# Optimization experiments

Measured on AMD Instinct MI355X. Metric: run time of the kernel, lower is better.

The kernel has to match this reference:

```python
import jax, jax.numpy as jnp
import numpy as np

H = 4096        # hidden_size
NH = 32         # num query heads
NG = 8          # num query groups (kv heads)
HD = H // NH    # head size = 128
B, S = 2, 2048


def gen_rope_cache(seq_length, n_elem, base=10000.0):
    theta = 1.0 / base ** (jnp.arange(0, n_elem, 2, dtype=jnp.float32) / n_elem)
    idx_theta = jnp.outer(jnp.arange(seq_length, dtype=jnp.float32), theta)
    return jnp.stack([jnp.cos(idx_theta), jnp.sin(idx_theta)], axis=-1)  # [S, n_elem//2, 2]


def apply_rope(x, cache):
    # x: [B, S, nh, hd], cache: [S, hd//2, 2]; rot_dim == hd (no pass-through)
    b, s, nh, hd = x.shape
    xr = x.reshape(b, s, nh, hd // 2, 2)
    c = cache[:s].reshape(1, s, 1, hd // 2, 2)
    out = jnp.stack([
        xr[..., 0] * c[..., 0] - xr[..., 1] * c[..., 1],
        xr[..., 1] * c[..., 0] + xr[..., 0] * c[..., 1],
    ], axis=-1)
    return out.reshape(b, s, nh, hd)


def setup_inputs() -> dict:
    key = jax.random.key(0)
    k1, k2, k3, k4 = jax.random.split(key, 4)
    x = jax.random.normal(k1, (B, S, H), dtype=jnp.float32)
    W_qkv = jax.random.normal(k2, (H, H + 2 * NG * HD), dtype=jnp.float32) * 0.02
    b_qkv = jax.random.normal(k3, (H + 2 * NG * HD,), dtype=jnp.float32) * 0.02
    W_dense = jax.random.normal(k4, (H, H), dtype=jnp.float32) * 0.02
    rope_cache = gen_rope_cache(S, HD)
    return {"x": x, "rope_cache": rope_cache, "W_qkv": W_qkv, "b_qkv": b_qkv, "W_dense": W_dense}


def reference(x, rope_cache, W_qkv, b_qkv, W_dense):
    b, s, h = x.shape
    qkv = jnp.einsum('bsh,ho->bso', x, W_qkv) + b_qkv
    q, k, v = jnp.split(qkv, [h, h + NG * HD], axis=-1)
    q = q.reshape(b, s, NH, HD)
    k = k.reshape(b, s, NG, HD)
    v = v.reshape(b, s, NG, HD)
    q = apply_rope(q, rope_cache)
    k = apply_rope(k, rope_cache)
    # GQA: group query heads [B, G, rep, S, D] against kv [B, G, S, D]
    rep = NH // NG
    qg = q.transpose(0, 2, 1, 3).reshape(b, NG, rep, s, HD)
    kg = k.transpose(0, 2, 1, 3)  # [B, G, S, D]
    vg = v.transpose(0, 2, 1, 3)
    scale = 1.0 / jnp.sqrt(jnp.float32(HD))
    scores = jnp.einsum('bgrqd,bgkd->bgrqk', qg, kg) * scale
    causal = jnp.tril(jnp.ones((s, s), dtype=bool))
    scores = jnp.where(causal, scores, jnp.float32(-1e30))
    attn = jax.nn.softmax(scores, axis=-1)
    out = jnp.einsum('bgrqk,bgkd->bgrqd', attn, vg)  # [B, G, rep, S, D]
    out = out.reshape(b, NH, s, HD).transpose(0, 2, 1, 3).reshape(b, s, h)
    return jnp.einsum('bsh,ho->bso', out, W_dense)
```

## Files before the change

### kernel.cpp

```cpp
#include <hip/hip_runtime.h>
#include <hip/hip_bf16.h>
#include <math.h>

#define BS   4096
#define HH   4096
#define NH   32
#define NG   8
#define HD   128
#define SEQ  2048
#define NQKV 6144

typedef float f32x4 __attribute__((ext_vector_type(4)));
typedef float f32x16 __attribute__((ext_vector_type(16)));
typedef short s16x8 __attribute__((ext_vector_type(8)));
typedef short s16x4 __attribute__((ext_vector_type(4)));
typedef unsigned int u32x4 __attribute__((ext_vector_type(4)));

__device__ __forceinline__ unsigned short f2bf(float f) {
  unsigned int u = __builtin_bit_cast(unsigned int, f);
  unsigned int r = (u + 0x7fffu + ((u >> 16) & 1u)) >> 16;
  return (unsigned short)r;
}
__device__ __forceinline__ float b2f(short h) {
  unsigned int u = ((unsigned int)(unsigned short)h) << 16;
  return __builtin_bit_cast(float, u);
}

__device__ __forceinline__ void gload16(const void* g, void* l) {
  __builtin_amdgcn_global_load_lds((__attribute__((address_space(1))) void*)(g),
                                   (__attribute__((address_space(3))) void*)(l), 16, 0, 0);
}

#define BARRIER __builtin_amdgcn_s_barrier()
#define PRIO1 __builtin_amdgcn_s_setprio(1)
#define PRIO0 __builtin_amdgcn_s_setprio(0)

__global__ void cast_f32_bf16(const float* __restrict__ in, short* __restrict__ out, long n4) {
  long i = (long)blockIdx.x * blockDim.x + threadIdx.x;
  long stride = (long)gridDim.x * blockDim.x;
  for (; i < n4; i += stride) {
    float4 v = *(const float4*)&in[i * 4];
    s16x4 o;
    o[0] = (short)f2bf(v.x); o[1] = (short)f2bf(v.y);
    o[2] = (short)f2bf(v.z); o[3] = (short)f2bf(v.w);
    *(s16x4*)&out[i * 4] = o;
  }
}

__global__ __launch_bounds__(256) void transpose_cast(const float* __restrict__ in,
                                                      short* __restrict__ out, int R, int C) {
  __shared__ float tile[32][33];
  int tx = threadIdx.x & 31, ty = threadIdx.x >> 5;
  long c0 = (long)blockIdx.x * 32, r0 = (long)blockIdx.y * 32;
#pragma unroll
  for (int j = 0; j < 32; j += 8)
    tile[ty + j][tx] = in[(r0 + ty + j) * C + c0 + tx];
  __syncthreads();
  int q = threadIdx.x & 7;
  int jj = threadIdx.x >> 3;
  s16x4 o;
  o[0] = (short)f2bf(tile[4 * q + 0][jj]);
  o[1] = (short)f2bf(tile[4 * q + 1][jj]);
  o[2] = (short)f2bf(tile[4 * q + 2][jj]);
  o[3] = (short)f2bf(tile[4 * q + 3][jj]);
  *(s16x4*)&out[(c0 + jj) * R + r0 + 4 * q] = o;
}

#define LDA_FR(BASE, DB)                                                         \
  {                                                                              \
    _Pragma("unroll") for (int mf = 0; mf < 4; ++mf)                             \
      _Pragma("unroll") for (int ks = 0; ks < 2; ++ks)                           \
        af[mf][ks] = *(const s16x8*)&lds[(BASE) + (DB) * 8192 + aoff[mf][ks]];   \
  }
#define LDB_FR(BASE, DB)                                                         \
  {                                                                              \
    _Pragma("unroll") for (int nf = 0; nf < 2; ++nf)                             \
      _Pragma("unroll") for (int ks = 0; ks < 2; ++ks)                           \
        bf[nf][ks] = *(const s16x8*)&lds[(BASE) + (DB) * 8192 + boff[nf][ks]];   \
  }
#define MF_Q(MS, NS)                                                             \
  {                                                                              \
    _Pragma("unroll") for (int ks = 0; ks < 2; ++ks)                             \
      _Pragma("unroll") for (int mf = 0; mf < 4; ++mf)                           \
        _Pragma("unroll") for (int nf = 0; nf < 2; ++nf)                         \
          acc[(MS) * 4 + mf][(NS) * 2 + nf] = __builtin_amdgcn_mfma_f32_16x16x32_bf16( \
              af[mf][ks], bf[nf][ks], acc[(MS) * 4 + mf][(NS) * 2 + nf], 0, 0, 0);     \
  }
#define STG_AU0(DB, KB) { gload16(sA0 + (KB), &lds[0 + (DB) * 8192 + du0]);            \
                          gload16(sA1 + (KB), &lds[0 + (DB) * 8192 + du1]); }
#define STG_BU0(DB, KB) { gload16(sB0 + (KB), &lds[32768 + (DB) * 8192 + du0]);        \
                          gload16(sB1 + (KB), &lds[32768 + (DB) * 8192 + du1]); }
#define STG_AU1(DB, KB) { gload16(sA0 + 64 * (long)K + (KB), &lds[16384 + (DB) * 8192 + du0]); \
                          gload16(sA1 + 64 * (long)K + (KB), &lds[16384 + (DB) * 8192 + du1]); }
#define STG_BU1(DB, KB) { gload16(sB0 + 32 * (long)K + (KB), &lds[49152 + (DB) * 8192 + du0]); \
                          gload16(sB1 + 32 * (long)K + (KB), &lds[49152 + (DB) * 8192 + du1]); }

#define TILE256(DB, KBS)                                                         \
  LDA_FR(0, DB); LDB_FR(32768, DB);                                              \
  STG_AU0(DB ^ 1, KBS); STG_BU0(DB ^ 1, KBS);                                    \
  BARRIER;                                                                       \
  PRIO1; MF_Q(0, 0); PRIO0;                                                      \
  asm volatile("s_waitcnt vmcnt(6)" ::: "memory");                               \
  BARRIER;                                                                       \
  LDB_FR(49152, DB);                                                             \
  STG_BU1(DB ^ 1, KBS);                                                          \
  BARRIER;                                                                       \
  PRIO1; MF_Q(0, 1); PRIO0;                                                      \
  asm volatile("s_waitcnt vmcnt(6)" ::: "memory");                               \
  BARRIER;                                                                       \
  LDA_FR(16384, DB);                                                             \
  STG_AU1(DB ^ 1, KBS);                                                          \
  BARRIER;                                                                       \
  PRIO1; MF_Q(1, 1); PRIO0;                                                      \
  BARRIER;                                                                       \
  LDB_FR(32768, DB);                                                             \
  BARRIER;                                                                       \
  PRIO1; MF_Q(1, 0); PRIO0;                                                      \
  asm volatile("s_waitcnt vmcnt(4)" ::: "memory");                               \
  BARRIER;

template <int MODE>
__global__ __launch_bounds__(512, 1) void gemm256(const short* __restrict__ A,
                                                  const short* __restrict__ Bt,
                                                  const float* __restrict__ bias,
                                                  void* __restrict__ Cout,
                                                  const float* __restrict__ cache,
                                                  short* __restrict__ Qb,
                                                  int M, int N, int K) {
  extern __shared__ short lds[];
  const int t = threadIdx.x;
  const int lane = t & 63, w = t >> 6;
  const int g = lane >> 4, lr = lane & 15;
  const int wm = w >> 2, wn = w & 3;
  const long bm = (long)blockIdx.y * 256;
  const long bn = (long)blockIdx.x * 256;

  const short *sA0, *sA1, *sB0, *sB1;
  {
    int c0 = t, c1 = t + 512;
    int h0 = c0 >> 9, r0 = (c0 >> 3) & 63, tc0 = (c0 & 7) ^ (r0 & 7);
    int h1 = c1 >> 9, r1 = (c1 >> 3) & 63, tc1 = (c1 & 7) ^ (r1 & 7);
    sA0 = A + (bm + h0 * 128 + r0) * (long)K + tc0 * 8;
    sA1 = A + (bm + h1 * 128 + r1) * (long)K + tc1 * 8;
    int g0 = c0 >> 8, rb0 = (c0 >> 3) & 31, tb0 = (c0 & 7) ^ (rb0 & 7);
    int g1 = c1 >> 8, rb1 = (c1 >> 3) & 31, tb1 = (c1 & 7) ^ (rb1 & 7);
    sB0 = Bt + (bn + g0 * 64 + rb0) * (long)K + tb0 * 8;
    sB1 = Bt + (bn + g1 * 64 + rb1) * (long)K + tb1 * 8;
  }
  const int du0 = w * 512;
  const int du1 = w * 512 + 4096;

  int aoff[4][2], boff[2][2];
#pragma unroll
  for (int mf = 0; mf < 4; ++mf)
#pragma unroll
    for (int ks = 0; ks < 2; ++ks)
      aoff[mf][ks] = wm * 4096 + (mf * 16 + lr) * 64 + (((ks * 4 + g) ^ (lr & 7)) * 8);
#pragma unroll
  for (int nf = 0; nf < 2; ++nf)
#pragma unroll
    for (int ks = 0; ks < 2; ++ks)
      boff[nf][ks] = wn * 2048 + (nf * 16 + lr) * 64 + (((ks * 4 + g) ^ (lr & 7)) * 8);

  f32x4 acc[8][4] = {};
  s16x8 af[4][2], bf[2][2];

  STG_AU0(0, 0); STG_BU0(0, 0); STG_AU1(0, 0); STG_BU1(0, 0);
  asm volatile("s_waitcnt vmcnt(0)" ::: "memory");
  BARRIER;

  const int NT = K >> 6;
  for (int kt = 0; kt < NT; kt += 2) {
    const long kb1 = (long)(kt + 1) * 64;
    const long kb2 = (kt + 2 < NT) ? (long)(kt + 2) * 64 : 0l;
    TILE256(0, kb1);
    TILE256(1, kb2);
  }

  if (MODE == 0) {
#pragma unroll
    for (int am = 0; am < 8; ++am) {
      long row = bm + wm * 128 + am * 16 + g * 4;
#pragma unroll
      for (int an = 0; an < 4; ++an) {
        long col = bn + wn * 64 + an * 16 + lr;
#pragma unroll
        for (int r = 0; r < 4; ++r)
          ((float*)Cout)[(row + r) * N + col] = acc[am][an][r];
      }
    }
  } else {
    const float scq = 0.12751743f;
#pragma unroll
    for (int am = 0; am < 8; ++am) {
      int row0 = (int)bm + wm * 128 + am * 16 + g * 4;
      int s0 = row0 & (SEQ - 1);
      int bb = row0 >> 11;
#pragma unroll
      for (int an = 0; an < 4; ++an) {
        int col = (int)bn + wn * 64 + an * 16 + lr;
        float bv = bias[col];
        int h = col >> 7, d = col & 127;
        const int odd = lr & 1;
#pragma unroll
        for (int r = 0; r < 4; ++r) {
          float v = acc[am][an][r] + bv;
          float p = __shfl_xor(v, 1);
          float2 cs = *(const float2*)&cache[((long)(s0 + r) * 64 + (d >> 1)) * 2];
          float o = odd ? (v * cs.x + p * cs.y) : (v * cs.x - p * cs.y);
          Qb[((long)(bb * NH + h) * SEQ + s0 + r) * HD + d] = (short)f2bf(o * scq);
        }
      }
    }
  }
}

#define KV_LDA(MSB, DB, KS)                                                      \
  { _Pragma("unroll") for (int mf = 0; mf < 4; ++mf)                             \
      af[mf] = *(const s16x8*)&lds[(MSB) + (DB) * 8192 + aoff[mf][KS]]; }
#define KV_LDB(DB, KS)                                                           \
  { _Pragma("unroll") for (int nf = 0; nf < 2; ++nf)                             \
      bfk[nf] = *(const s16x8*)&lds[32768 + (DB) * 8192 + boff[nf][KS]]; }
#define KV_MF(MS)                                                                \
  { _Pragma("unroll") for (int mf = 0; mf < 4; ++mf)                             \
      _Pragma("unroll") for (int nf = 0; nf < 2; ++nf)                           \
        acc[(MS) * 4 + mf][nf] = __builtin_amdgcn_mfma_f32_16x16x32_bf16(        \
            af[mf], bfk[nf], acc[(MS) * 4 + mf][nf], 0, 0, 0); }
#define KV_SA0(DB, KB) { gload16(sA0 + (KB), &lds[(DB) * 8192 + du0]);                 \
                         gload16(sA1 + (KB), &lds[(DB) * 8192 + du1]); }
#define KV_SA1(DB, KB) { gload16(sA0 + 64 * (long)HH + (KB), &lds[16384 + (DB) * 8192 + du0]); \
                         gload16(sA1 + 64 * (long)HH + (KB), &lds[16384 + (DB) * 8192 + du1]); }
#define KV_SB(DB, KB)  { gload16(sB0 + (KB), &lds[32768 + (DB) * 8192 + du0]);         \
                         gload16(sB1 + (KB), &lds[32768 + (DB) * 8192 + du1]); }

#define KVTILE(DB, KBS)                                                          \
  KV_LDA(0, DB, 0); KV_LDB(DB, 0);                                               \
  KV_SA0(DB ^ 1, KBS);                                                           \
  BARRIER;                                                                       \
  PRIO1; KV_MF(0); PRIO0;                                                        \
  asm volatile("s_waitcnt vmcnt(2)" ::: "memory");                               \
  BARRIER;                                                                       \
  KV_LDA(16384, DB, 0);                                                          \
  KV_SB(DB ^ 1, KBS);                                                            \
  BARRIER;                                                                       \
  PRIO1; KV_MF(1); PRIO0;                                                        \
  BARRIER;                                                                       \
  KV_LDA(16384, DB, 1); KV_LDB(DB, 1);                                           \
  KV_SA1(DB ^ 1, KBS);                                                           \
  BARRIER;                                                                       \
  PRIO1; KV_MF(1); PRIO0;                                                        \
  BARRIER;                                                                       \
  KV_LDA(0, DB, 1);                                                              \
  BARRIER;                                                                       \
  PRIO1; KV_MF(0); PRIO0;                                                        \
  asm volatile("s_waitcnt vmcnt(2)" ::: "memory");                               \
  BARRIER;

__global__ __launch_bounds__(512, 1) void gemm_kv(const short* __restrict__ A,
                                                  const short* __restrict__ Bt,
                                                  const float* __restrict__ bias,
                                                  const float* __restrict__ cache,
                                                  short* __restrict__ Kb,
                                                  short* __restrict__ Vtb) {
  extern __shared__ short lds[];
  const int t = threadIdx.x;
  const int lane = t & 63, w = t >> 6;
  const int g = lane >> 4, lr = lane & 15;
  const int wm = w >> 2, wn = w & 3;
  const long bm = (long)blockIdx.y * 256;
  const int bnl = blockIdx.x * 128;

  const short *sA0, *sA1, *sB0, *sB1;
  {
    int c0 = t, c1 = t + 512;
    int h0 = c0 >> 9, r0 = (c0 >> 3) & 63, tc0 = (c0 & 7) ^ (r0 & 7);
    int h1 = c1 >> 9, r1 = (c1 >> 3) & 63, tc1 = (c1 & 7) ^ (r1 & 7);
    sA0 = A + (bm + h0 * 128 + r0) * (long)HH + tc0 * 8;
    sA1 = A + (bm + h1 * 128 + r1) * (long)HH + tc1 * 8;
    int rb0 = c0 >> 3, tb0 = (c0 & 7) ^ (rb0 & 7);
    int rb1 = c1 >> 3, tb1 = (c1 & 7) ^ (rb1 & 7);
    sB0 = Bt + ((long)bnl + rb0) * HH + tb0 * 8;
    sB1 = Bt + ((long)bnl + rb1) * HH + tb1 * 8;
  }
  const int du0 = w * 512;
  const int du1 = w * 512 + 4096;

  int aoff[4][2], boff[2][2];
#pragma unroll
  for (int mf = 0; mf < 4; ++mf)
#pragma unroll
    for (int ks = 0; ks < 2; ++ks)
      aoff[mf][ks] = wm * 4096 + (mf * 16 + lr) * 64 + (((ks * 4 + g) ^ (lr & 7)) * 8);
#pragma unroll
  for (int nf = 0; nf < 2; ++nf)
#pragma unroll
    for (int ks = 0; ks < 2; ++ks)
      boff[nf][ks] = wn * 2048 + (nf * 16 + lr) * 64 + (((ks * 4 + g) ^ (lr & 7)) * 8);

  f32x4 acc[8][2] = {};
  s16x8 af[4], bfk[2];

  KV_SA0(0, 0); KV_SB(0, 0); KV_SA1(0, 0);
  asm volatile("s_waitcnt vmcnt(0)" ::: "memory");
  BARRIER;

  for (int kt = 0; kt < 64; kt += 2) {
    const long kb1 = (long)(kt + 1) * 64;
    const long kb2 = (kt + 2 < 64) ? (long)(kt + 2) * 64 : 0l;
    KVTILE(0, kb1);
    KVTILE(1, kb2);
  }

#pragma unroll
  for (int am = 0; am < 8; ++am) {
    int row0 = (int)bm + wm * 128 + am * 16 + g * 4;
    int s0 = row0 & (SEQ - 1);
    int bb = row0 >> 11;
#pragma unroll
    for (int an = 0; an < 2; ++an) {
      int cl = bnl + wn * 32 + an * 16 + lr;
      float bv = bias[4096 + cl];
      if (cl < 1024) {
        int gi = cl >> 7, d = cl & 127;
        const int odd = lr & 1;
#pragma unroll
        for (int r = 0; r < 4; ++r) {
          float v = acc[am][an][r] + bv;
          float p = __shfl_xor(v, 1);
          float2 cs = *(const float2*)&cache[((long)(s0 + r) * 64 + (d >> 1)) * 2];
          float o = odd ? (v * cs.x + p * cs.y) : (v * cs.x - p * cs.y);
          Kb[((long)(bb * NG + gi) * SEQ + s0 + r) * HD + d] = (short)f2bf(o);
        }
      } else {
        int cv = cl - 1024;
        int gi = cv >> 7, d = cv & 127;
        s16x4 o;
#pragma unroll
        for (int r = 0; r < 4; ++r) o[r] = (short)f2bf(acc[am][an][r] + bv);
        *(s16x4*)&Vtb[((long)(bb * NG + gi) * HD + d) * SEQ + s0] = o;
      }
    }
  }
}

__global__ __launch_bounds__(512, 1) void attn(const short* __restrict__ Qb,
                                               const short* __restrict__ Kb,
                                               const short* __restrict__ Vtb,
                                               short* __restrict__ Ob) {
  extern __shared__ short alds[];
  const int t = threadIdx.x, lane = t & 63, w = t >> 6;
  const int l31 = lane & 31, hi = lane >> 5;
  const int bid = (int)blockIdx.x;
  const int q0 = (bid >> 1) & 3;
  const int qt = ((bid ^ (bid >> 8)) & 1) ? 7 - q0 : q0;
  const int head = (bid >> 3) & 63;
  const int b = head >> 5, h = head & 31;
  const int qb = qt * 256;
  const short* Qhead = Qb + (long)(b * NH + h) * SEQ * HD;
  const short* Khead = Kb + (long)(b * NG + (h >> 2)) * SEQ * HD;
  const short* Vthead = Vtb + (long)(b * NG + (h >> 2)) * SEQ * HD;
  const int qw0 = qb + w * 32;
  const int qrow = qw0 + l31;
  float* facs = (float*)&alds[32768] + w * 32;

  s16x8 qf[8];
#pragma unroll
  for (int ds = 0; ds < 8; ++ds)
    qf[ds] = *(const s16x8*)&Qhead[(long)qrow * HD + ds * 16 + hi * 8];

  const short *kp0, *kp1, *vp0, *vp1;
  {
    int c0 = t, c1 = t + 512;
    int kr0 = c0 >> 4, kc0 = (c0 & 15) ^ (kr0 & 15);
    int kr1 = c1 >> 4, kc1 = (c1 & 15) ^ (kr1 & 15);
    kp0 = Khead + (long)kr0 * HD + kc0 * 8;
    kp1 = Khead + (long)kr1 * HD + kc1 * 8;
    int vr0 = c0 >> 3, vc0 = (c0 & 7) ^ (vr0 & 7);
    int vr1 = c1 >> 3, vc1 = (c1 & 7) ^ (vr1 & 7);
    vp0 = Vthead + (long)vr0 * SEQ + vc0 * 8;
    vp1 = Vthead + (long)vr1 * SEQ + vc1 * 8;
  }
  const int d0 = w * 512, d1 = w * 512 + 4096;

  f32x16 ao[4] = {};
  float mrun = -1.0e30f, lrun = 0.0f;
  const int nkt = 4 * qt + 4;

  gload16(kp0, &alds[d0]); gload16(kp1, &alds[d1]);
  gload16(vp0, &alds[16384 + d0]); gload16(vp1, &alds[16384 + d1]);
  kp0 += 64 * HD; kp1 += 64 * HD; vp0 += 64; vp1 += 64;
  asm volatile("s_waitcnt vmcnt(0)" ::: "memory");
  BARRIER;

  for (int kt = 0; kt < nkt; ++kt) {
    const int buf = kt & 1, nb = buf ^ 1;
    const int kb = kt * 64;
    const int bK = buf * 8192, bV = 16384 + buf * 8192;
    if (kt + 1 < nkt) {
      gload16(kp0, &alds[nb * 8192 + d0]); gload16(kp1, &alds[nb * 8192 + d1]);
      gload16(vp0, &alds[16384 + nb * 8192 + d0]); gload16(vp1, &alds[16384 + nb * 8192 + d1]);
      kp0 += 64 * HD; kp1 += 64 * HD; vp0 += 64; vp1 += 64;
    }
    if (kb <= qw0 + 31) {
      f32x16 st0 = {}, st1 = {};
#pragma unroll
      for (int ds = 0; ds < 8; ++ds) {
        const int c = ds * 2 + hi;
        const int r0 = l31, r1 = 32 + l31;
        s16x8 kf0 = *(const s16x8*)&alds[bK + r0 * 128 + ((c ^ (r0 & 15)) * 8)];
        s16x8 kf1 = *(const s16x8*)&alds[bK + r1 * 128 + ((c ^ (r1 & 15)) * 8)];
        st0 = __builtin_amdgcn_mfma_f32_32x32x16_bf16(kf0, qf[ds], st0, 0, 0, 0);
        st1 = __builtin_amdgcn_mfma_f32_32x32x16_bf16(kf1, qf[ds], st1, 0, 0, 0);
      }

      float p[32];
      if (kb + 63 > qrow || kb + 63 > qw0) {
#pragma unroll
        for (int r = 0; r < 16; ++r) {
          int kg = kb + (r & 3) + 8 * (r >> 2) + 4 * hi;
          p[r] = (kg > qrow) ? -1.0e30f : st0[r];
          p[16 + r] = (kg + 32 > qrow) ? -1.0e30f : st1[r];
        }
      } else {
#pragma unroll
        for (int r = 0; r < 16; ++r) { p[r] = st0[r]; p[16 + r] = st1[r]; }
      }
      float tt[16];
#pragma unroll
      for (int i = 0; i < 16; ++i) tt[i] = fmaxf(p[i], p[i + 16]);
#pragma unroll
      for (int s = 8; s >= 1; s >>= 1)
#pragma unroll
        for (int i = 0; i < 8; ++i)
          if (i < s) tt[i] = fmaxf(tt[i], tt[i + s]);
      float tmax = tt[0];
      tmax = fmaxf(tmax, __shfl_xor(tmax, 32));
      if (!__all(tmax <= mrun + 8.0f)) {
        float mnew = fmaxf(mrun, tmax);
        float fac = exp2f(mrun - mnew);
        facs[l31] = fac;
        mrun = mnew; lrun *= fac;
        f32x4 f0 = *(f32x4*)&facs[0 + 4 * hi];
        f32x4 f1 = *(f32x4*)&facs[8 + 4 * hi];
        f32x4 f2 = *(f32x4*)&facs[16 + 4 * hi];
        f32x4 f3 = *(f32x4*)&facs[24 + 4 * hi];
#pragma unroll
        for (int j = 0; j < 4; ++j)
#pragma unroll
          for (int dt = 0; dt < 4; ++dt) {
            ao[dt][j] *= f0[j]; ao[dt][4 + j] *= f1[j];
            ao[dt][8 + j] *= f2[j]; ao[dt][12 + j] *= f3[j];
          }
      }
#pragma unroll
      for (int i = 0; i < 32; ++i) p[i] = exp2f(p[i] - mrun);
      float ss[16];
#pragma unroll
      for (int i = 0; i < 16; ++i) ss[i] = p[i] + p[i + 16];
#pragma unroll
      for (int s = 8; s >= 1; s >>= 1)
#pragma unroll
        for (int i = 0; i < 8; ++i)
          if (i < s) ss[i] = ss[i] + ss[i + s];
      float tsum = ss[0];
      lrun += tsum + __shfl_xor(tsum, 32);

      s16x8 pa[4];
#pragma unroll
      for (int ks = 0; ks < 4; ++ks) {
        unsigned w0, w1, w2, w3;
        asm("v_cvt_pk_bf16_f32 %0, %1, %2" : "=v"(w0) : "v"(p[ks * 8 + 0]), "v"(p[ks * 8 + 1]));
        asm("v_cvt_pk_bf16_f32 %0, %1, %2" : "=v"(w1) : "v"(p[ks * 8 + 2]), "v"(p[ks * 8 + 3]));
        asm("v_cvt_pk_bf16_f32 %0, %1, %2" : "=v"(w2) : "v"(p[ks * 8 + 4]), "v"(p[ks * 8 + 5]));
        asm("v_cvt_pk_bf16_f32 %0, %1, %2" : "=v"(w3) : "v"(p[ks * 8 + 6]), "v"(p[ks * 8 + 7]));
        unsigned sw0 = (unsigned)__shfl_xor((int)w0, 32);
        unsigned sw1 = (unsigned)__shfl_xor((int)w1, 32);
        unsigned sw2 = (unsigned)__shfl_xor((int)w2, 32);
        unsigned sw3 = (unsigned)__shfl_xor((int)w3, 32);
        u32x4 pw;
        pw[0] = hi ? sw2 : w0;
        pw[1] = hi ? sw3 : w1;
        pw[2] = hi ? w2 : sw0;
        pw[3] = hi ? w3 : sw1;
        pa[ks] = __builtin_bit_cast(s16x8, pw);
      }

#pragma unroll
      for (int ks = 0; ks < 4; ++ks)
#pragma unroll
        for (int dt = 0; dt < 4; ++dt) {
          int dd = dt * 32 + l31;
          int slot = (ks * 2 + hi) ^ (dd & 7);
          s16x8 vf = *(const s16x8*)&alds[bV + dd * 64 + slot * 8];
          ao[dt] = __builtin_amdgcn_mfma_f32_32x32x16_bf16(pa[ks], vf, ao[dt], 0, 0, 0);
        }
    }
    asm volatile("s_waitcnt vmcnt(0)" ::: "memory");
    BARRIER;
  }

  facs[l31] = 1.0f / lrun;
  float invr[16];
  {
    f32x4 i0 = *(f32x4*)&facs[0 + 4 * hi];
    f32x4 i1 = *(f32x4*)&facs[8 + 4 * hi];
    f32x4 i2 = *(f32x4*)&facs[16 + 4 * hi];
    f32x4 i3 = *(f32x4*)&facs[24 + 4 * hi];
#pragma unroll
    for (int j = 0; j < 4; ++j) {
      invr[j] = i0[j]; invr[4 + j] = i1[j]; invr[8 + j] = i2[j]; invr[12 + j] = i3[j];
    }
  }
#pragma unroll
  for (int dt = 0; dt < 4; ++dt)
#pragma unroll
    for (int r = 0; r < 16; ++r) {
      int grow = qw0 + (r & 3) + 8 * (r >> 2) + 4 * hi;
      Ob[((long)b * SEQ + grow) * HH + h * HD + dt * 32 + l31] = (short)f2bf(ao[dt][r] * invr[r]);
    }
}

extern "C" void kernel_launch(void* const* d_in, const int* in_sizes, int n_in,
                              void* d_out, int out_size, void* d_ws, size_t ws_size,
                              hipStream_t stream) {
  const float* x     = (const float*)d_in[0];
  const float* cache = (const float*)d_in[1];
  const float* Wqkv  = (const float*)d_in[2];
  const float* bqkv  = (const float*)d_in[3];
  const float* Wd    = (const float*)d_in[4];

  char* ws = (char*)d_ws;
  short* xb   = (short*)(ws);
  short* wqt  = (short*)(ws + 33554432ll);
  short* wdt  = (short*)(ws + 83886080ll);
  short* Qb   = (short*)(ws + 167772160ll);
  short* Kb   = (short*)(ws + 201326592ll);
  short* Vtb  = (short*)(ws + 218103808ll);
  short* Ob   = (short*)(ws + 226492416ll);

  cast_f32_bf16<<<2048, 256, 0, stream>>>(x, xb, (long)BS * HH / 4);
  transpose_cast<<<dim3(NQKV / 32, HH / 32), 256, 0, stream>>>(Wqkv, wqt, HH, NQKV);
  transpose_cast<<<dim3(HH / 32, HH / 32), 256, 0, stream>>>(Wd, wdt, HH, HH);
  gemm256<2><<<dim3(16, 16), 512, 131072, stream>>>(
      xb, wqt, bqkv, nullptr, cache, Qb, BS, HH, HH);
  gemm_kv<<<dim3(16, 16), 512, 98304, stream>>>(
      xb, wqt + 4096ll * HH, bqkv, cache, Kb, Vtb);
  attn<<<512, 512, 66560, stream>>>(Qb, Kb, Vtb, Ob);
  gemm256<0><<<dim3(16, 16), 512, 131072, stream>>>(
      Ob, wdt, nullptr, d_out, nullptr, nullptr, BS, HH, HH);
}
```

Before: 487.4 us.

## Remap attention block order for KV-group locality, add MFMA priority, use permlane32 swap

Rewrites the block-index decode so that blocks sharing a KV group and batch are grouped together, with causal tile pairing (qt and 7-qt) kept, to improve L2 reuse of K/V across concurrently running blocks. It also raises wave priority around the two MFMA loops (PRIO1/PRIO0), and replaces four cross-half shuffles plus selects with two v_permlane32_swap instructions when packing P into bf16 fragments. The remap changes which blocks run together and so affects load balance. Correctness depends on the new mapping covering every (b, h, qt) exactly once.

```diff
diff --git a/kernel.cpp b/kernel.cpp
--- a/kernel.cpp
+++ b/kernel.cpp
@@ -351,10 +351,15 @@
   const int t = threadIdx.x, lane = t & 63, w = t >> 6;
   const int l31 = lane & 31, hi = lane >> 5;
   const int bid = (int)blockIdx.x;
-  const int q0 = (bid >> 1) & 3;
-  const int qt = ((bid ^ (bid >> 8)) & 1) ? 7 - q0 : q0;
-  const int head = (bid >> 3) & 63;
-  const int b = head >> 5, h = head & 31;
+  const int gg = bid & 15;
+  const int j  = bid >> 4;
+  const int p_ = j & 1;
+  const int a_ = j >> 1;
+  const int q0 = a_ & 7;
+  const int h2 = a_ >> 3;
+  const int qt = p_ ? 7 - q0 : q0;
+  const int b  = gg >> 3;
+  const int h  = (gg & 7) * 4 + h2 * 2 + p_;
   const int qb = qt * 256;
   const short* Qhead = Qb + (long)(b * NH + h) * SEQ * HD;
   const short* Khead = Kb + (long)(b * NG + (h >> 2)) * SEQ * HD;
@@ -403,6 +408,7 @@
     }
     if (kb <= qw0 + 31) {
       f32x16 st0 = {}, st1 = {};
+      PRIO1;
 #pragma unroll
       for (int ds = 0; ds < 8; ++ds) {
         const int c = ds * 2 + hi;
@@ -412,6 +418,7 @@
         st0 = __builtin_amdgcn_mfma_f32_32x32x16_bf16(kf0, qf[ds], st0, 0, 0, 0);
         st1 = __builtin_amdgcn_mfma_f32_32x32x16_bf16(kf1, qf[ds], st1, 0, 0, 0);
       }
+      PRIO0;
 
       float p[32];
       if (kb + 63 > qrow || kb + 63 > qw0) {
@@ -445,11 +452,11 @@
         f32x4 f2 = *(f32x4*)&facs[16 + 4 * hi];
         f32x4 f3 = *(f32x4*)&facs[24 + 4 * hi];
 #pragma unroll
-        for (int j = 0; j < 4; ++j)
+        for (int j2 = 0; j2 < 4; ++j2)
 #pragma unroll
           for (int dt = 0; dt < 4; ++dt) {
-            ao[dt][j] *= f0[j]; ao[dt][4 + j] *= f1[j];
-            ao[dt][8 + j] *= f2[j]; ao[dt][12 + j] *= f3[j];
+            ao[dt][j2] *= f0[j2]; ao[dt][4 + j2] *= f1[j2];
+            ao[dt][8 + j2] *= f2[j2]; ao[dt][12 + j2] *= f3[j2];
           }
       }
 #pragma unroll
@@ -473,18 +480,14 @@
         asm("v_cvt_pk_bf16_f32 %0, %1, %2" : "=v"(w1) : "v"(p[ks * 8 + 2]), "v"(p[ks * 8 + 3]));
         asm("v_cvt_pk_bf16_f32 %0, %1, %2" : "=v"(w2) : "v"(p[ks * 8 + 4]), "v"(p[ks * 8 + 5]));
         asm("v_cvt_pk_bf16_f32 %0, %1, %2" : "=v"(w3) : "v"(p[ks * 8 + 6]), "v"(p[ks * 8 + 7]));
-        unsigned sw0 = (unsigned)__shfl_xor((int)w0, 32);
-        unsigned sw1 = (unsigned)__shfl_xor((int)w1, 32);
-        unsigned sw2 = (unsigned)__shfl_xor((int)w2, 32);
-        unsigned sw3 = (unsigned)__shfl_xor((int)w3, 32);
+        asm("v_permlane32_swap_b32 %0, %1" : "+v"(w0), "+v"(w2));
+        asm("v_permlane32_swap_b32 %0, %1" : "+v"(w1), "+v"(w3));
         u32x4 pw;
-        pw[0] = hi ? sw2 : w0;
-        pw[1] = hi ? sw3 : w1;
-        pw[2] = hi ? w2 : sw0;
-        pw[3] = hi ? w3 : sw1;
+        pw[0] = w0; pw[1] = w1; pw[2] = w2; pw[3] = w3;
         pa[ks] = __builtin_bit_cast(s16x8, pw);
       }
 
+      PRIO1;
 #pragma unroll
       for (int ks = 0; ks < 4; ++ks)
 #pragma unroll
@@ -494,6 +497,7 @@
           s16x8 vf = *(const s16x8*)&alds[bV + dd * 64 + slot * 8];
           ao[dt] = __builtin_amdgcn_mfma_f32_32x32x16_bf16(pa[ks], vf, ao[dt], 0, 0, 0);
         }
+      PRIO0;
     }
     asm volatile("s_waitcnt vmcnt(0)" ::: "memory");
     BARRIER;
@@ -507,8 +511,8 @@
     f32x4 i2 = *(f32x4*)&facs[16 + 4 * hi];
     f32x4 i3 = *(f32x4*)&facs[24 + 4 * hi];
 #pragma unroll
-    for (int j = 0; j < 4; ++j) {
-      invr[j] = i0[j]; invr[4 + j] = i1[j]; invr[8 + j] = i2[j]; invr[12 + j] = i3[j];
+    for (int j2 = 0; j2 < 4; ++j2) {
+      invr[j2] = i0[j2]; invr[4 + j2] = i1[j2]; invr[8 + j2] = i2[j2]; invr[12 + j2] = i3[j2];
     }
   }
 #pragma unroll
```

After: 529.0 us. 1.09x slower.
